# Performance work log

Hardware: AMD Instinct MI355X
Metric: run time of the kernel (lower is better)

## Reference

```python
import jax, jax.numpy as jnp
import numpy as np

C = 1024
H = 16
D = C // H

def setup_inputs() -> dict:
    key = jax.random.key(0)
    ks = jax.random.split(key, 12)
    s = 1.0 / np.sqrt(C)
    inp = {
        "Q": jax.random.normal(ks[0], (2, 1024, C), jnp.float32),
        "K_in": jax.random.normal(ks[1], (2, 4096, C), jnp.float32),
        "V_in": jax.random.normal(ks[2], (2, 4096, C), jnp.float32),
        "V_bias": jax.random.normal(ks[3], (2, 4096), jnp.float32),
        "Wq_w": jax.random.uniform(ks[4], (C, C), jnp.float32, -s, s),
        "Wq_b": jax.random.uniform(ks[5], (C,), jnp.float32, -s, s),
        "Wk_w": jax.random.uniform(ks[6], (C, C), jnp.float32, -s, s),
        "Wk_b": jax.random.uniform(ks[7], (C,), jnp.float32, -s, s),
        "Wv_w": jax.random.uniform(ks[8], (C, C), jnp.float32, -s, s),
        "Wv_b": jax.random.uniform(ks[9], (C,), jnp.float32, -s, s),
        "Wo_w": jax.random.uniform(ks[10], (C, C), jnp.float32, -s, s),
        "Wo_b": jax.random.uniform(ks[11], (C,), jnp.float32, -s, s),
    }
    return inp

def reference(Q, K_in, V_in, V_bias, Wq_w, Wq_b, Wk_w, Wk_b, Wv_w, Wv_b, Wo_w, Wo_b):
    B, Lq, _ = Q.shape
    Lk = K_in.shape[1]
    # linear projections (torch Linear: x @ W.T + b), split heads -> [B,H,L,D]
    q = (Q @ Wq_w.T + Wq_b).reshape(B, Lq, H, D).transpose(0, 2, 1, 3)
    k = (K_in @ Wk_w.T + Wk_b).reshape(B, Lk, H, D).transpose(0, 2, 1, 3)
    v = (V_in @ Wv_w.T + Wv_b).reshape(B, Lk, H, D).transpose(0, 2, 1, 3)
    scale = 1.0 / np.sqrt(D).astype(np.float32)
    logits = jnp.einsum("bhqd,bhkd->bhqk", q, k) * scale
    logits = logits + V_bias[:, None, None, :]  # per-key additive bias
    attn = jax.nn.softmax(logits, axis=-1)      # dropout p=0.0 (eval)
    out = jnp.einsum("bhqk,bhkd->bhqd", attn, v)
    out = out.transpose(0, 2, 1, 3).reshape(B, Lq, C)
    return out @ Wo_w.T + Wo_b
```

## Files before the change

### kernel.cpp

```cpp
#include <hip/hip_runtime.h>


typedef __attribute__((ext_vector_type(8))) __bf16 bf16x8;
typedef __attribute__((ext_vector_type(4))) float f32x4;
typedef __attribute__((ext_vector_type(16))) float f32x16;

#define LOG2E 1.44269504f

__device__ __forceinline__ unsigned short f2bf(float f) {
  union { float f; unsigned u; } v; v.f = f;
  unsigned r = v.u + 0x7fffu + ((v.u >> 16) & 1u);
  return (unsigned short)(r >> 16);
}
__device__ __forceinline__ unsigned short f2h(float x) {
  _Float16 h = (_Float16)x;
  return __builtin_bit_cast(unsigned short, h);
}
__device__ __forceinline__ float h2f(unsigned short u) {
  return (float)__builtin_bit_cast(_Float16, u);
}

__device__ __forceinline__ f32x4 mfma16(bf16x8 a, bf16x8 b, f32x4 c) {
  return __builtin_amdgcn_mfma_f32_16x16x32_bf16(a, b, c, 0, 0, 0);
}
__device__ __forceinline__ f32x16 mfma32(bf16x8 a, bf16x8 b, f32x16 c) {
  return __builtin_amdgcn_mfma_f32_32x32x16_bf16(a, b, c, 0, 0, 0);
}

__device__ __forceinline__ unsigned pk2(float lo, float hi) {
  unsigned short a = __builtin_bit_cast(unsigned short, (__bf16)lo);
  unsigned short b = __builtin_bit_cast(unsigned short, (__bf16)hi);
  return (unsigned)a | ((unsigned)b << 16);
}

template <typename T>
__device__ __forceinline__ void gload16(const T* g, T* l) {
  __builtin_amdgcn_global_load_lds(
      (const __attribute__((address_space(1))) void*)g,
      (__attribute__((address_space(3))) void*)l, 16, 0, 0);
}

struct Cvt4 {
  const float* src[4];
  unsigned short* dst[4];
};

__global__ __launch_bounds__(256) void cvt4_kernel(Cvt4 a, int n4) {
  const float4* s = (const float4*)a.src[blockIdx.y];
  unsigned short* d = a.dst[blockIdx.y];
  int stride = gridDim.x * blockDim.x;
  for (int i = blockIdx.x * blockDim.x + threadIdx.x; i < n4; i += stride) {
    float4 f = s[i];
    ushort4 u;
    u.x = f2bf(f.x); u.y = f2bf(f.y); u.z = f2bf(f.z); u.w = f2bf(f.w);
    ((ushort4*)d)[i] = u;
  }
}

__global__ __launch_bounds__(256) void prep_kb(const float* __restrict__ Vb,
                                               unsigned* __restrict__ kb) {
  const int i = blockIdx.x * 256 + threadIdx.x;
  const float x = Vb[i] * LOG2E;
  const unsigned short h = f2bf(x);
  union { unsigned u; float f; } hf; hf.u = (unsigned)h << 16;
  const unsigned short lo = f2bf(x - hf.f);
  kb[i] = (unsigned)h | ((unsigned)lo << 16);
}

template <int MODE, bool AF32>
__global__ __launch_bounds__(256) void gemm_bf16(
    const void* __restrict__ Ap, const unsigned short* __restrict__ W,
    const float* __restrict__ bias, void* __restrict__ outp,
    int M, int Llog2, float oscale) {
  constexpr int K = 1024, N = 1024;
  __shared__ unsigned short Alds[128][40];
  __shared__ unsigned short Blds[128][40];

  const int tid = threadIdx.x;
  const int wid = tid >> 6, l = tid & 63;
  const int wr = wid >> 1, wc = wid & 1;
  const int m0 = blockIdx.x * 128, n0 = blockIdx.y * 128;
  const int lg = l >> 4, lm = l & 15;

  const int crow = tid >> 2;
  const int ck8 = (tid & 3) * 8;

  const float* Af = (const float*)Ap;
  const unsigned short* Ab = (const unsigned short*)Ap;

  f32x4 acc[4][4] = {};
  uint4 ra[2], rb[2];

  auto loadA = [&](int kt, int half) -> uint4 {
    const int row = crow + half * 64;
    const long off = (long)(m0 + row) * K + kt * 32 + ck8;
    if constexpr (AF32) {
      float4 f0 = *(const float4*)(Af + off);
      float4 f1 = *(const float4*)(Af + off + 4);
      bf16x8 v;
      v[0] = (__bf16)f0.x; v[1] = (__bf16)f0.y;
      v[2] = (__bf16)f0.z; v[3] = (__bf16)f0.w;
      v[4] = (__bf16)f1.x; v[5] = (__bf16)f1.y;
      v[6] = (__bf16)f1.z; v[7] = (__bf16)f1.w;
      uint4 u;
      __builtin_memcpy(&u, &v, 16);
      return u;
    } else {
      return *(const uint4*)(Ab + off);
    }
  };
  auto loadB = [&](int kt, int half) -> uint4 {
    const int row = crow + half * 64;
    return *(const uint4*)(W + (long)(n0 + row) * K + kt * 32 + ck8);
  };

  ra[0] = loadA(0, 0); ra[1] = loadA(0, 1);
  rb[0] = loadB(0, 0); rb[1] = loadB(0, 1);

  for (int kt = 0; kt < K / 32; ++kt) {
    __syncthreads();
    *(uint4*)&Alds[crow][ck8] = ra[0];
    *(uint4*)&Alds[crow + 64][ck8] = ra[1];
    *(uint4*)&Blds[crow][ck8] = rb[0];
    *(uint4*)&Blds[crow + 64][ck8] = rb[1];
    __syncthreads();
    if (kt + 1 < K / 32) {
      ra[0] = loadA(kt + 1, 0); ra[1] = loadA(kt + 1, 1);
      rb[0] = loadB(kt + 1, 0); rb[1] = loadB(kt + 1, 1);
    }
    bf16x8 af[4], bfr[4];
#pragma unroll
    for (int i = 0; i < 4; ++i)
      af[i] = *(const bf16x8*)&Alds[wr * 64 + i * 16 + lm][lg * 8];
#pragma unroll
    for (int j = 0; j < 4; ++j)
      bfr[j] = *(const bf16x8*)&Blds[wc * 64 + j * 16 + lm][lg * 8];
#pragma unroll
    for (int i = 0; i < 4; ++i)
#pragma unroll
      for (int j = 0; j < 4; ++j) {
        if constexpr (MODE == 1)
          acc[i][j] = mfma16(bfr[i], af[j], acc[i][j]);
        else
          acc[i][j] = mfma16(af[i], bfr[j], acc[i][j]);
      }
  }

  const int rr = lg * 4;
  if constexpr (MODE == 0) {
    const int Lmask = (1 << Llog2) - 1;
    unsigned short* out = (unsigned short*)outp;
#pragma unroll
    for (int j = 0; j < 4; ++j) {
      const int n = n0 + wc * 64 + j * 16 + lm;
      const float bv = bias[n];
      const int h = n >> 6, d = n & 63;
#pragma unroll
      for (int i = 0; i < 4; ++i)
#pragma unroll
        for (int r = 0; r < 4; ++r) {
          const int m = m0 + wr * 64 + i * 16 + rr + r;
          const int b = m >> Llog2, li = m & Lmask;
          const long o = (((long)(b * 16 + h) << Llog2) + li) * 64 + d;
          out[o] = f2bf((acc[i][j][r] + bv) * oscale);
        }
    }
  } else if constexpr (MODE == 1) {
    unsigned short* out = (unsigned short*)outp;
#pragma unroll
    for (int i = 0; i < 4; ++i)
#pragma unroll
      for (int r = 0; r < 4; ++r) {
        const int n = n0 + wc * 64 + i * 16 + rr + r;
        const float bv = bias[n];
        const int h = n >> 6, d = n & 63;
#pragma unroll
        for (int j = 0; j < 4; ++j) {
          const int m = m0 + wr * 64 + j * 16 + lm;
          const int b = m >> 12, lk = m & 4095;
          const long o = ((long)((b * 16 + h) * 64 + d)) * 4096 + lk;
          out[o] = f2bf(acc[i][j][r] + bv);
        }
      }
  } else {
    float* out = (float*)outp;
#pragma unroll
    for (int j = 0; j < 4; ++j) {
      const int n = n0 + wc * 64 + j * 16 + lm;
      const float bv = bias[n];
#pragma unroll
      for (int i = 0; i < 4; ++i)
#pragma unroll
        for (int r = 0; r < 4; ++r) {
          const int m = m0 + wr * 64 + i * 16 + rr + r;
          out[(long)m * N + n] = acc[i][j][r] + bv;
        }
    }
  }
}

__global__ __launch_bounds__(256, 3) void attn32(
    const unsigned short* __restrict__ qh, const unsigned short* __restrict__ kh,
    const unsigned short* __restrict__ vT, const unsigned* __restrict__ kb,
    unsigned short* __restrict__ Oh, float* __restrict__ ml) {
  __shared__ unsigned short Klds[2][64][64];
  __shared__ unsigned short Vlds[2][64][64];

  const int tid = threadIdx.x;
  const int wid = tid >> 6, lane = tid & 63;
  const int lq = lane & 31, hi = lane >> 5;
  const int bh = blockIdx.x, qb = blockIdx.y, sp = blockIdx.z;
  const int b = bh >> 4;
  const int q = qb * 128 + wid * 32 + lq;
  const int kt0 = sp * 16;

  bf16x8 qr[4];
  {
    const unsigned short* qp = qh + ((long)bh * 1024 + q) * 64 + hi * 8;
#pragma unroll
    for (int dc = 0; dc < 4; ++dc) qr[dc] = *(const bf16x8*)(qp + dc * 16);
  }

  union uv { uint4 u; bf16x8 v; };
  uv ones; ones.u = make_uint4(0x3F803F80u, 0x3F803F80u, 0x3F803F80u, 0x3F803F80u);
  uv bq;   bq.u = make_uint4(hi ? 0u : 0x3F803F80u, 0u, 0u, 0u);

  auto swap23 = [](int r) { return (r & 0x33) | ((r & 4) << 1) | ((r & 8) >> 1); };
  const int r0 = wid * 16 + (lane >> 3), r1 = r0 + 8;
  const int s0 = ((lane & 7) ^ (r0 & 7)) * 8;
  const int s1 = ((lane & 7) ^ (r1 & 7)) * 8;
  const unsigned short* kg0 =
      kh + ((long)bh * 4096 + kt0 * 64 + swap23(r0)) * 64 + s0;
  const unsigned short* kg1 =
      kh + ((long)bh * 4096 + kt0 * 64 + swap23(r1)) * 64 + s1;
  const unsigned short* vg0 = vT + ((long)bh * 64 + r0) * 4096 + kt0 * 64 + s0;
  const unsigned short* vg1 = vT + ((long)bh * 64 + r1) * 4096 + kt0 * 64 + s1;
  const unsigned* kbp = kb + b * 4096 + kt0 * 64;
  const int kbkey = swap23(lq);

  auto issue = [&](int t, int buf) {
    gload16(kg0 + (long)t * 4096, &Klds[buf][wid * 16][0]);
    gload16(kg1 + (long)t * 4096, &Klds[buf][wid * 16 + 8][0]);
    gload16(vg0 + t * 64, &Vlds[buf][wid * 16][0]);
    gload16(vg1 + t * 64, &Vlds[buf][wid * 16 + 8][0]);
  };
  issue(0, 0);

  const int rsw = lq & 7;
  float mreg = -1e30f;
  f32x16 oa0 = {}, oa1 = {}, lacc = {};

  for (int t = 0; t < 16; ++t) {
    const int buf = t & 1;
    __syncthreads();
    if (t + 1 < 16) issue(t + 1, buf ^ 1);

    const unsigned kbw0 = kbp[t * 64 + kbkey];
    const unsigned kbw1 = kbp[t * 64 + 32 + kbkey];

    f32x16 sa0 = {}, sa1 = {};
    __builtin_amdgcn_s_setprio(1);
#pragma unroll
    for (int dc = 0; dc < 4; ++dc) {
      const int so = ((dc * 2 + hi) ^ rsw) * 8;
      bf16x8 kf0 = *(const bf16x8*)&Klds[buf][lq][so];
      bf16x8 kf1 = *(const bf16x8*)&Klds[buf][32 + lq][so];
      sa0 = mfma32(kf0, qr[dc], sa0);
      sa1 = mfma32(kf1, qr[dc], sa1);
    }
    {
      uv ka0, ka1;
      ka0.u = make_uint4(hi ? 0u : kbw0, 0u, 0u, 0u);
      ka1.u = make_uint4(hi ? 0u : kbw1, 0u, 0u, 0u);
      sa0 = mfma32(ka0.v, bq.v, sa0);
      sa1 = mfma32(ka1.v, bq.v, sa1);
    }
    __builtin_amdgcn_s_setprio(0);

    float p[32];
#pragma unroll
    for (int r = 0; r < 16; ++r) { p[r] = sa0[r]; p[16 + r] = sa1[r]; }

    float t8[8];
#pragma unroll
    for (int i = 0; i < 8; ++i)
      t8[i] = fmaxf(fmaxf(p[i], p[i + 8]), fmaxf(p[i + 16], p[i + 24]));
    float mx = fmaxf(fmaxf(fmaxf(t8[0], t8[1]), fmaxf(t8[2], t8[3])),
                     fmaxf(fmaxf(t8[4], t8[5]), fmaxf(t8[6], t8[7])));
    mx = fmaxf(mx, __shfl_xor(mx, 32));

    if (!__all(mx - mreg <= 8.0f)) {
      const float mnew = fmaxf(mreg, mx);
      const float al = __builtin_amdgcn_exp2f(mreg - mnew);
      mreg = mnew;
#pragma unroll
      for (int r = 0; r < 16; ++r) { oa0[r] *= al; oa1[r] *= al; }
      lacc[0] *= al;
    }
#pragma unroll
    for (int i = 0; i < 32; ++i) p[i] = __builtin_amdgcn_exp2f(p[i] - mreg);

    __builtin_amdgcn_s_setprio(1);
#pragma unroll
    for (int kc = 0; kc < 4; ++kc) {
      uv pu;
      pu.u = make_uint4(pk2(p[kc * 8 + 0], p[kc * 8 + 1]),
                        pk2(p[kc * 8 + 2], p[kc * 8 + 3]),
                        pk2(p[kc * 8 + 4], p[kc * 8 + 5]),
                        pk2(p[kc * 8 + 6], p[kc * 8 + 7]));
      const int so = ((kc * 2 + hi) ^ rsw) * 8;
      bf16x8 vf0 = *(const bf16x8*)&Vlds[buf][lq][so];
      bf16x8 vf1 = *(const bf16x8*)&Vlds[buf][32 + lq][so];
      oa0 = mfma32(vf0, pu.v, oa0);
      oa1 = mfma32(vf1, pu.v, oa1);
      lacc = mfma32(ones.v, pu.v, lacc);
    }
    __builtin_amdgcn_s_setprio(0);
  }

  const float lsum = lacc[0];
  const float inv = 1.0f / lsum;
  unsigned short* ob = Oh + (((long)sp * 32 + bh) * 1024 + q) * 64 + hi * 4;
#pragma unroll
  for (int g = 0; g < 4; ++g) {
    ushort4 u0, u1;
    u0.x = f2h(oa0[g * 4 + 0] * inv); u0.y = f2h(oa0[g * 4 + 1] * inv);
    u0.z = f2h(oa0[g * 4 + 2] * inv); u0.w = f2h(oa0[g * 4 + 3] * inv);
    u1.x = f2h(oa1[g * 4 + 0] * inv); u1.y = f2h(oa1[g * 4 + 1] * inv);
    u1.z = f2h(oa1[g * 4 + 2] * inv); u1.w = f2h(oa1[g * 4 + 3] * inv);
    *(ushort4*)(ob + g * 8) = u0;
    *(ushort4*)(ob + 32 + g * 8) = u1;
  }
  if (hi == 0)
    *(float2*)(ml + (((long)sp * 32 + bh) * 1024 + q) * 2) =
        make_float2(mreg, lsum);
}

__global__ __launch_bounds__(256) void combine4(
    const unsigned short* __restrict__ Oh, const float* __restrict__ ml,
    unsigned short* __restrict__ ao) {
  const int idx = blockIdx.x * 256 + threadIdx.x;
  const int bh = idx >> 10, q = idx & 1023;
  const int b = bh >> 4, h = bh & 15;
  float m[4], l[4];
#pragma unroll
  for (int i = 0; i < 4; ++i) {
    float2 t = *(const float2*)(ml + ((long)i * 32768 + idx) * 2);
    m[i] = t.x; l[i] = t.y;
  }
  const float mm = fmaxf(fmaxf(m[0], m[1]), fmaxf(m[2], m[3]));
  float w[4], wsum = 0.f;
#pragma unroll
  for (int i = 0; i < 4; ++i) {
    w[i] = l[i] * __builtin_amdgcn_exp2f(m[i] - mm);
    wsum += w[i];
  }
  const float inv = 1.0f / wsum;
#pragma unroll
  for (int i = 0; i < 4; ++i) w[i] *= inv;

  unsigned short* op = ao + ((long)b * 1024 + q) * 1024 + h * 64;
#pragma unroll
  for (int blk = 0; blk < 8; ++blk) {
    float acc[8] = {};
#pragma unroll
    for (int i = 0; i < 4; ++i) {
      uint4 u = *(const uint4*)(Oh + ((long)i * 32768 + idx) * 64 + blk * 8);
      const unsigned short* hs = (const unsigned short*)&u;
#pragma unroll
      for (int j = 0; j < 8; ++j) acc[j] += w[i] * h2f(hs[j]);
    }
    ushort4 o0, o1;
    o0.x = f2bf(acc[0]); o0.y = f2bf(acc[1]);
    o0.z = f2bf(acc[2]); o0.w = f2bf(acc[3]);
    o1.x = f2bf(acc[4]); o1.y = f2bf(acc[5]);
    o1.z = f2bf(acc[6]); o1.w = f2bf(acc[7]);
    *(ushort4*)(op + blk * 8) = o0;
    *(ushort4*)(op + blk * 8 + 4) = o1;
  }
}

extern "C" void kernel_launch(void* const* d_in, const int* in_sizes, int n_in,
                              void* d_out, int out_size, void* d_ws,
                              size_t ws_size, hipStream_t stream) {
  const float* Q = (const float*)d_in[0];
  const float* K_in = (const float*)d_in[1];
  const float* V_in = (const float*)d_in[2];
  const float* V_bias = (const float*)d_in[3];
  const float* Wq_w = (const float*)d_in[4];
  const float* Wq_b = (const float*)d_in[5];
  const float* Wk_w = (const float*)d_in[6];
  const float* Wk_b = (const float*)d_in[7];
  const float* Wv_w = (const float*)d_in[8];
  const float* Wv_b = (const float*)d_in[9];
  const float* Wo_w = (const float*)d_in[10];
  const float* Wo_b = (const float*)d_in[11];

  char* ws = (char*)d_ws;
  unsigned short* Wqb = (unsigned short*)(ws + (0l << 20));
  float* mlp = (float*)(ws + (0l << 20));
  unsigned short* Wkb = (unsigned short*)(ws + (2l << 20));
  unsigned short* Wvb = (unsigned short*)(ws + (4l << 20));
  unsigned short* Wob = (unsigned short*)(ws + (6l << 20));
  unsigned short* qhp = (unsigned short*)(ws + (8l << 20));
  unsigned short* khp = (unsigned short*)(ws + (12l << 20));
  unsigned short* vTp = (unsigned short*)(ws + (28l << 20));
  unsigned short* Ohp = (unsigned short*)(ws + (44l << 20));
  unsigned short* aop = (unsigned short*)(ws + (60l << 20));
  unsigned* kbp = (unsigned*)(ws + (64l << 20));

  Cvt4 c4;
  c4.src[0] = Wq_w; c4.src[1] = Wk_w; c4.src[2] = Wv_w; c4.src[3] = Wo_w;
  c4.dst[0] = Wqb;  c4.dst[1] = Wkb;  c4.dst[2] = Wvb;  c4.dst[3] = Wob;
  cvt4_kernel<<<dim3(256, 4), 256, 0, stream>>>(c4, (1024 * 1024) / 4);
  prep_kb<<<32, 256, 0, stream>>>(V_bias, kbp);

  gemm_bf16<0, true><<<dim3(16, 8), 256, 0, stream>>>(
      Q, Wqb, Wq_b, qhp, 2048, 10, 0.125f * LOG2E);
  gemm_bf16<0, true><<<dim3(64, 8), 256, 0, stream>>>(
      K_in, Wkb, Wk_b, khp, 8192, 12, 1.0f);
  gemm_bf16<1, true><<<dim3(64, 8), 256, 0, stream>>>(
      V_in, Wvb, Wv_b, vTp, 8192, 12, 1.0f);

  attn32<<<dim3(32, 8, 4), 256, 0, stream>>>(qhp, khp, vTp, kbp, Ohp, mlp);
  combine4<<<128, 256, 0, stream>>>(Ohp, mlp, aop);

  gemm_bf16<2, false><<<dim3(16, 8), 256, 0, stream>>>(
      aop, Wob, Wo_b, d_out, 2048, 0, 1.0f);
}
```

Measured before the change: 188.7 us.

## Restructure GEMM loads and double query tile per warp in attention

The projection GEMM now reads A straight from global memory into registers in MFMA fragment layout, and stages B with async global-to-LDS loads into a double buffer with a single barrier per k-step. A 64-row tile variant is added for the small Q and output GEMMs so they launch more blocks. The attention kernel gives each warp 64 queries as two interleaved 32-query groups that share K/V fragments, which improves reuse and overlaps softmax with MFMA. The row sum is now computed with a register reduction instead of an extra ones-vector MFMA. In exchange, register pressure rises, occupancy hints drop from 3 to 2, and the attention grid halves, leaving fewer waves on the GPU.

After: 285.4 us. 1.51x slower.

```diff
diff --git a/kernel.cpp b/kernel.cpp
--- a/kernel.cpp
+++ b/kernel.cpp
@@ -67,83 +67,95 @@
   kb[i] = (unsigned)h | ((unsigned)lo << 16);
 }
 
-template <int MODE, bool AF32>
-__global__ __launch_bounds__(256) void gemm_bf16(
+template <int MODE, bool AF32, int BM>
+__global__ __launch_bounds__(256, 2) void gemm_bf16(
     const void* __restrict__ Ap, const unsigned short* __restrict__ W,
     const float* __restrict__ bias, void* __restrict__ outp,
-    int M, int Llog2, float oscale) {
+    int Llog2, float oscale) {
   constexpr int K = 1024, N = 1024;
-  __shared__ unsigned short Alds[128][40];
-  __shared__ unsigned short Blds[128][40];
+  constexpr int NJ = (BM == 128) ? 4 : 2;
+  __shared__ unsigned short Blds[2][128][32];
 
   const int tid = threadIdx.x;
   const int wid = tid >> 6, l = tid & 63;
-  const int wr = wid >> 1, wc = wid & 1;
-  const int m0 = blockIdx.x * 128, n0 = blockIdx.y * 128;
   const int lg = l >> 4, lm = l & 15;
-
-  const int crow = tid >> 2;
-  const int ck8 = (tid & 3) * 8;
+  const int wr = (BM == 128) ? (wid >> 1) : 0;
+  const int wc = (BM == 128) ? (wid & 1) : wid;
+  const int m0 = blockIdx.x * BM, n0 = blockIdx.y * 128;
+  const int mbase = m0 + wr * 64;
+  const int nbase = (BM == 128) ? wc * 64 : wid * 32;
 
   const float* Af = (const float*)Ap;
   const unsigned short* Ab = (const unsigned short*)Ap;
 
-  f32x4 acc[4][4] = {};
-  uint4 ra[2], rb[2];
-
-  auto loadA = [&](int kt, int half) -> uint4 {
-    const int row = crow + half * 64;
-    const long off = (long)(m0 + row) * K + kt * 32 + ck8;
-    if constexpr (AF32) {
-      float4 f0 = *(const float4*)(Af + off);
-      float4 f1 = *(const float4*)(Af + off + 4);
-      bf16x8 v;
-      v[0] = (__bf16)f0.x; v[1] = (__bf16)f0.y;
-      v[2] = (__bf16)f0.z; v[3] = (__bf16)f0.w;
-      v[4] = (__bf16)f1.x; v[5] = (__bf16)f1.y;
-      v[6] = (__bf16)f1.z; v[7] = (__bf16)f1.w;
-      uint4 u;
-      __builtin_memcpy(&u, &v, 16);
-      return u;
-    } else {
-      return *(const uint4*)(Ab + off);
+  const int bidx = wid * 1024 + (tid & 63) * 16;
+  const int brow = bidx >> 6;
+  const int bcol = (bidx & 63) >> 1;
+  const unsigned short* bsrc0 = W + (long)(n0 + brow) * K + bcol;
+  const unsigned short* bsrc1 = W + (long)(n0 + 64 + brow) * K + bcol;
+
+  f32x4 acc[4][NJ] = {};
+  uint4 pa[4][2];
+
+  auto loadA = [&](int kt) {
+#pragma unroll
+    for (int i = 0; i < 4; ++i) {
+      const long off = (long)(mbase + i * 16 + lm) * K + kt * 32 + lg * 8;
+      if constexpr (AF32) {
+        pa[i][0] = *(const uint4*)(Af + off);
+        pa[i][1] = *(const uint4*)(Af + off + 4);
+      } else {
+        pa[i][0] = *(const uint4*)(Ab + off);
+      }
     }
   };
-  auto loadB = [&](int kt, int half) -> uint4 {
-    const int row = crow + half * 64;
-    return *(const uint4*)(W + (long)(n0 + row) * K + kt * 32 + ck8);
+  auto issueB = [&](int kt, int buf) {
+    gload16(bsrc0 + kt * 32, &Blds[buf][wid * 16][0]);
+    gload16(bsrc1 + kt * 32, &Blds[buf][64 + wid * 16][0]);
   };
 
-  ra[0] = loadA(0, 0); ra[1] = loadA(0, 1);
-  rb[0] = loadB(0, 0); rb[1] = loadB(0, 1);
+  issueB(0, 0);
+  loadA(0);
 
   for (int kt = 0; kt < K / 32; ++kt) {
+    const int buf = kt & 1;
     __syncthreads();
-    *(uint4*)&Alds[crow][ck8] = ra[0];
-    *(uint4*)&Alds[crow + 64][ck8] = ra[1];
-    *(uint4*)&Blds[crow][ck8] = rb[0];
-    *(uint4*)&Blds[crow + 64][ck8] = rb[1];
-    __syncthreads();
-    if (kt + 1 < K / 32) {
-      ra[0] = loadA(kt + 1, 0); ra[1] = loadA(kt + 1, 1);
-      rb[0] = loadB(kt + 1, 0); rb[1] = loadB(kt + 1, 1);
-    }
-    bf16x8 af[4], bfr[4];
+    if (kt + 1 < K / 32) issueB(kt + 1, buf ^ 1);
+
+    bf16x8 af[4];
+#pragma unroll
+    for (int i = 0; i < 4; ++i) {
+      if constexpr (AF32) {
+        union { uint4 u[2]; float f[8]; } t;
+        t.u[0] = pa[i][0]; t.u[1] = pa[i][1];
+        bf16x8 v;
+#pragma unroll
+        for (int e = 0; e < 8; ++e) v[e] = (__bf16)t.f[e];
+        af[i] = v;
+      } else {
+        union { uint4 u; bf16x8 v; } t;
+        t.u = pa[i][0];
+        af[i] = t.v;
+      }
+    }
+    if (kt + 1 < K / 32) loadA(kt + 1);
+
+    bf16x8 bfr[NJ];
+#pragma unroll
+    for (int j = 0; j < NJ; ++j)
+      bfr[j] = *(const bf16x8*)&Blds[buf][nbase + j * 16 + lm][lg * 8];
+
+    __builtin_amdgcn_s_setprio(1);
 #pragma unroll
     for (int i = 0; i < 4; ++i)
-      af[i] = *(const bf16x8*)&Alds[wr * 64 + i * 16 + lm][lg * 8];
-#pragma unroll
-    for (int j = 0; j < 4; ++j)
-      bfr[j] = *(const bf16x8*)&Blds[wc * 64 + j * 16 + lm][lg * 8];
-#pragma unroll
-    for (int i = 0; i < 4; ++i)
-#pragma unroll
-      for (int j = 0; j < 4; ++j) {
+#pragma unroll
+      for (int j = 0; j < NJ; ++j) {
         if constexpr (MODE == 1)
-          acc[i][j] = mfma16(bfr[i], af[j], acc[i][j]);
+          acc[i][j] = mfma16(bfr[j], af[i], acc[i][j]);
         else
           acc[i][j] = mfma16(af[i], bfr[j], acc[i][j]);
       }
+    __builtin_amdgcn_s_setprio(0);
   }
 
   const int rr = lg * 4;
@@ -151,15 +163,15 @@
     const int Lmask = (1 << Llog2) - 1;
     unsigned short* out = (unsigned short*)outp;
 #pragma unroll
-    for (int j = 0; j < 4; ++j) {
-      const int n = n0 + wc * 64 + j * 16 + lm;
+    for (int j = 0; j < NJ; ++j) {
+      const int n = n0 + nbase + j * 16 + lm;
       const float bv = bias[n];
       const int h = n >> 6, d = n & 63;
 #pragma unroll
       for (int i = 0; i < 4; ++i)
 #pragma unroll
         for (int r = 0; r < 4; ++r) {
-          const int m = m0 + wr * 64 + i * 16 + rr + r;
+          const int m = mbase + i * 16 + rr + r;
           const int b = m >> Llog2, li = m & Lmask;
           const long o = (((long)(b * 16 + h) << Llog2) + li) * 64 + d;
           out[o] = f2bf((acc[i][j][r] + bv) * oscale);
@@ -171,35 +183,35 @@
     for (int i = 0; i < 4; ++i)
 #pragma unroll
       for (int r = 0; r < 4; ++r) {
-        const int n = n0 + wc * 64 + i * 16 + rr + r;
+        const int n = n0 + nbase + i * 16 + rr + r;
         const float bv = bias[n];
         const int h = n >> 6, d = n & 63;
 #pragma unroll
         for (int j = 0; j < 4; ++j) {
-          const int m = m0 + wr * 64 + j * 16 + lm;
+          const int m = mbase + j * 16 + lm;
           const int b = m >> 12, lk = m & 4095;
           const long o = ((long)((b * 16 + h) * 64 + d)) * 4096 + lk;
-          out[o] = f2bf(acc[i][j][r] + bv);
+          out[o] = f2bf(acc[j][i][r] + bv);
         }
       }
   } else {
     float* out = (float*)outp;
 #pragma unroll
-    for (int j = 0; j < 4; ++j) {
-      const int n = n0 + wc * 64 + j * 16 + lm;
+    for (int j = 0; j < NJ; ++j) {
+      const int n = n0 + nbase + j * 16 + lm;
       const float bv = bias[n];
 #pragma unroll
       for (int i = 0; i < 4; ++i)
 #pragma unroll
         for (int r = 0; r < 4; ++r) {
-          const int m = m0 + wr * 64 + i * 16 + rr + r;
+          const int m = mbase + i * 16 + rr + r;
           out[(long)m * N + n] = acc[i][j][r] + bv;
         }
     }
   }
 }
 
-__global__ __launch_bounds__(256, 3) void attn32(
+__global__ __launch_bounds__(256, 2) void attn64(
     const unsigned short* __restrict__ qh, const unsigned short* __restrict__ kh,
     const unsigned short* __restrict__ vT, const unsigned* __restrict__ kb,
     unsigned short* __restrict__ Oh, float* __restrict__ ml) {
@@ -211,19 +223,21 @@
   const int lq = lane & 31, hi = lane >> 5;
   const int bh = blockIdx.x, qb = blockIdx.y, sp = blockIdx.z;
   const int b = bh >> 4;
-  const int q = qb * 128 + wid * 32 + lq;
+  const int qA = qb * 256 + wid * 64 + lq;
   const int kt0 = sp * 16;
 
-  bf16x8 qr[4];
+  bf16x8 qrA[4], qrB[4];
   {
-    const unsigned short* qp = qh + ((long)bh * 1024 + q) * 64 + hi * 8;
-#pragma unroll
-    for (int dc = 0; dc < 4; ++dc) qr[dc] = *(const bf16x8*)(qp + dc * 16);
+    const unsigned short* qp = qh + ((long)bh * 1024 + qA) * 64 + hi * 8;
+#pragma unroll
+    for (int dc = 0; dc < 4; ++dc) {
+      qrA[dc] = *(const bf16x8*)(qp + dc * 16);
+      qrB[dc] = *(const bf16x8*)(qp + 32 * 64 + dc * 16);
+    }
   }
 
   union uv { uint4 u; bf16x8 v; };
-  uv ones; ones.u = make_uint4(0x3F803F80u, 0x3F803F80u, 0x3F803F80u, 0x3F803F80u);
-  uv bq;   bq.u = make_uint4(hi ? 0u : 0x3F803F80u, 0u, 0u, 0u);
+  uv bq; bq.u = make_uint4(hi ? 0u : 0x3F803F80u, 0u, 0u, 0u);
 
   auto swap23 = [](int r) { return (r & 0x33) | ((r & 4) << 1) | ((r & 8) >> 1); };
   const int r0 = wid * 16 + (lane >> 3), r1 = r0 + 8;
@@ -247,40 +261,15 @@
   issue(0, 0);
 
   const int rsw = lq & 7;
-  float mreg = -1e30f;
-  f32x16 oa0 = {}, oa1 = {}, lacc = {};
-
-  for (int t = 0; t < 16; ++t) {
-    const int buf = t & 1;
-    __syncthreads();
-    if (t + 1 < 16) issue(t + 1, buf ^ 1);
-
-    const unsigned kbw0 = kbp[t * 64 + kbkey];
-    const unsigned kbw1 = kbp[t * 64 + 32 + kbkey];
-
-    f32x16 sa0 = {}, sa1 = {};
-    __builtin_amdgcn_s_setprio(1);
-#pragma unroll
-    for (int dc = 0; dc < 4; ++dc) {
-      const int so = ((dc * 2 + hi) ^ rsw) * 8;
-      bf16x8 kf0 = *(const bf16x8*)&Klds[buf][lq][so];
-      bf16x8 kf1 = *(const bf16x8*)&Klds[buf][32 + lq][so];
-      sa0 = mfma32(kf0, qr[dc], sa0);
-      sa1 = mfma32(kf1, qr[dc], sa1);
-    }
-    {
-      uv ka0, ka1;
-      ka0.u = make_uint4(hi ? 0u : kbw0, 0u, 0u, 0u);
-      ka1.u = make_uint4(hi ? 0u : kbw1, 0u, 0u, 0u);
-      sa0 = mfma32(ka0.v, bq.v, sa0);
-      sa1 = mfma32(ka1.v, bq.v, sa1);
-    }
-    __builtin_amdgcn_s_setprio(0);
-
+  float mA = -1e30f, mB = -1e30f, lA = 0.f, lB = 0.f;
+  f32x16 oaA0 = {}, oaA1 = {}, oaB0 = {}, oaB1 = {};
+  uv puA[4], puB[4];
+
+  auto softmax = [&](f32x16& sx0, f32x16& sx1, float& mreg, float& lreg,
+                     f32x16& o0, f32x16& o1, uv* pu) {
     float p[32];
 #pragma unroll
-    for (int r = 0; r < 16; ++r) { p[r] = sa0[r]; p[16 + r] = sa1[r]; }
-
+    for (int r = 0; r < 16; ++r) { p[r] = sx0[r]; p[16 + r] = sx1[r]; }
     float t8[8];
 #pragma unroll
     for (int i = 0; i < 8; ++i)
@@ -288,52 +277,118 @@
     float mx = fmaxf(fmaxf(fmaxf(t8[0], t8[1]), fmaxf(t8[2], t8[3])),
                      fmaxf(fmaxf(t8[4], t8[5]), fmaxf(t8[6], t8[7])));
     mx = fmaxf(mx, __shfl_xor(mx, 32));
-
     if (!__all(mx - mreg <= 8.0f)) {
       const float mnew = fmaxf(mreg, mx);
       const float al = __builtin_amdgcn_exp2f(mreg - mnew);
       mreg = mnew;
 #pragma unroll
-      for (int r = 0; r < 16; ++r) { oa0[r] *= al; oa1[r] *= al; }
-      lacc[0] *= al;
+      for (int r = 0; r < 16; ++r) { o0[r] *= al; o1[r] *= al; }
+      lreg *= al;
     }
 #pragma unroll
     for (int i = 0; i < 32; ++i) p[i] = __builtin_amdgcn_exp2f(p[i] - mreg);
-
+    float s16[16];
+#pragma unroll
+    for (int i = 0; i < 16; ++i) s16[i] = p[i] + p[i + 16];
+#pragma unroll
+    for (int s = 8; s > 0; s >>= 1)
+#pragma unroll
+      for (int i = 0; i < 8; ++i)
+        if (i < s) s16[i] += s16[i + s];
+    lreg += s16[0] + __shfl_xor(s16[0], 32);
+#pragma unroll
+    for (int kc = 0; kc < 4; ++kc)
+      pu[kc].u = make_uint4(pk2(p[kc * 8 + 0], p[kc * 8 + 1]),
+                            pk2(p[kc * 8 + 2], p[kc * 8 + 3]),
+                            pk2(p[kc * 8 + 4], p[kc * 8 + 5]),
+                            pk2(p[kc * 8 + 6], p[kc * 8 + 7]));
+  };
+
+  for (int t = 0; t < 16; ++t) {
+    const int buf = t & 1;
+    __syncthreads();
+    if (t + 1 < 16) issue(t + 1, buf ^ 1);
+
+    uv ka0, ka1;
+    ka0.u = make_uint4(hi ? 0u : kbp[t * 64 + kbkey], 0u, 0u, 0u);
+    ka1.u = make_uint4(hi ? 0u : kbp[t * 64 + 32 + kbkey], 0u, 0u, 0u);
+
+    bf16x8 kf0[4], kf1[4];
+#pragma unroll
+    for (int dc = 0; dc < 4; ++dc) {
+      const int so = ((dc * 2 + hi) ^ rsw) * 8;
+      kf0[dc] = *(const bf16x8*)&Klds[buf][lq][so];
+      kf1[dc] = *(const bf16x8*)&Klds[buf][32 + lq][so];
+    }
+
+    f32x16 sa0 = {}, sa1 = {};
     __builtin_amdgcn_s_setprio(1);
 #pragma unroll
+    for (int dc = 0; dc < 4; ++dc) {
+      sa0 = mfma32(kf0[dc], qrA[dc], sa0);
+      sa1 = mfma32(kf1[dc], qrA[dc], sa1);
+    }
+    sa0 = mfma32(ka0.v, bq.v, sa0);
+    sa1 = mfma32(ka1.v, bq.v, sa1);
+    __builtin_amdgcn_s_setprio(0);
+    softmax(sa0, sa1, mA, lA, oaA0, oaA1, puA);
+
+    f32x16 sb0 = {}, sb1 = {};
+    __builtin_amdgcn_s_setprio(1);
+#pragma unroll
+    for (int dc = 0; dc < 4; ++dc) {
+      sb0 = mfma32(kf0[dc], qrB[dc], sb0);
+      sb1 = mfma32(kf1[dc], qrB[dc], sb1);
+    }
+    sb0 = mfma32(ka0.v, bq.v, sb0);
+    sb1 = mfma32(ka1.v, bq.v, sb1);
+    __builtin_amdgcn_s_setprio(0);
+
+    bf16x8 vf0[4], vf1[4];
+#pragma unroll
     for (int kc = 0; kc < 4; ++kc) {
-      uv pu;
-      pu.u = make_uint4(pk2(p[kc * 8 + 0], p[kc * 8 + 1]),
-                        pk2(p[kc * 8 + 2], p[kc * 8 + 3]),
-                        pk2(p[kc * 8 + 4], p[kc * 8 + 5]),
-                        pk2(p[kc * 8 + 6], p[kc * 8 + 7]));
       const int so = ((kc * 2 + hi) ^ rsw) * 8;
-      bf16x8 vf0 = *(const bf16x8*)&Vlds[buf][lq][so];
-      bf16x8 vf1 = *(const bf16x8*)&Vlds[buf][32 + lq][so];
-      oa0 = mfma32(vf0, pu.v, oa0);
-      oa1 = mfma32(vf1, pu.v, oa1);
-      lacc = mfma32(ones.v, pu.v, lacc);
+      vf0[kc] = *(const bf16x8*)&Vlds[buf][lq][so];
+      vf1[kc] = *(const bf16x8*)&Vlds[buf][32 + lq][so];
+    }
+    softmax(sb0, sb1, mB, lB, oaB0, oaB1, puB);
+
+    __builtin_amdgcn_s_setprio(1);
+#pragma unroll
+    for (int kc = 0; kc < 4; ++kc) {
+      oaA0 = mfma32(vf0[kc], puA[kc].v, oaA0);
+      oaA1 = mfma32(vf1[kc], puA[kc].v, oaA1);
+      oaB0 = mfma32(vf0[kc], puB[kc].v, oaB0);
+      oaB1 = mfma32(vf1[kc], puB[kc].v, oaB1);
     }
     __builtin_amdgcn_s_setprio(0);
   }
 
-  const float lsum = lacc[0];
-  const float inv = 1.0f / lsum;
-  unsigned short* ob = Oh + (((long)sp * 32 + bh) * 1024 + q) * 64 + hi * 4;
+  const float invA = 1.0f / lA, invB = 1.0f / lB;
+  unsigned short* obA = Oh + (((long)sp * 32 + bh) * 1024 + qA) * 64 + hi * 4;
+  unsigned short* obB = obA + 32 * 64;
 #pragma unroll
   for (int g = 0; g < 4; ++g) {
-    ushort4 u0, u1;
-    u0.x = f2h(oa0[g * 4 + 0] * inv); u0.y = f2h(oa0[g * 4 + 1] * inv);
-    u0.z = f2h(oa0[g * 4 + 2] * inv); u0.w = f2h(oa0[g * 4 + 3] * inv);
-    u1.x = f2h(oa1[g * 4 + 0] * inv); u1.y = f2h(oa1[g * 4 + 1] * inv);
-    u1.z = f2h(oa1[g * 4 + 2] * inv); u1.w = f2h(oa1[g * 4 + 3] * inv);
-    *(ushort4*)(ob + g * 8) = u0;
-    *(ushort4*)(ob + 32 + g * 8) = u1;
-  }
-  if (hi == 0)
-    *(float2*)(ml + (((long)sp * 32 + bh) * 1024 + q) * 2) =
-        make_float2(mreg, lsum);
+    ushort4 u;
+    u.x = f2h(oaA0[g * 4 + 0] * invA); u.y = f2h(oaA0[g * 4 + 1] * invA);
+    u.z = f2h(oaA0[g * 4 + 2] * invA); u.w = f2h(oaA0[g * 4 + 3] * invA);
+    *(ushort4*)(obA + g * 8) = u;
+    u.x = f2h(oaA1[g * 4 + 0] * invA); u.y = f2h(oaA1[g * 4 + 1] * invA);
+    u.z = f2h(oaA1[g * 4 + 2] * invA); u.w = f2h(oaA1[g * 4 + 3] * invA);
+    *(ushort4*)(obA + 32 + g * 8) = u;
+    u.x = f2h(oaB0[g * 4 + 0] * invB); u.y = f2h(oaB0[g * 4 + 1] * invB);
+    u.z = f2h(oaB0[g * 4 + 2] * invB); u.w = f2h(oaB0[g * 4 + 3] * invB);
+    *(ushort4*)(obB + g * 8) = u;
+    u.x = f2h(oaB1[g * 4 + 0] * invB); u.y = f2h(oaB1[g * 4 + 1] * invB);
+    u.z = f2h(oaB1[g * 4 + 2] * invB); u.w = f2h(oaB1[g * 4 + 3] * invB);
+    *(ushort4*)(obB + 32 + g * 8) = u;
+  }
+  if (hi == 0) {
+    *(float2*)(ml + (((long)sp * 32 + bh) * 1024 + qA) * 2) =
+        make_float2(mA, lA);
+    *(float2*)(ml + (((long)sp * 32 + bh) * 1024 + qA + 32) * 2) =
+        make_float2(mB, lB);
+  }
 }
 
 __global__ __launch_bounds__(256) void combine4(
@@ -415,16 +470,16 @@
   cvt4_kernel<<<dim3(256, 4), 256, 0, stream>>>(c4, (1024 * 1024) / 4);
   prep_kb<<<32, 256, 0, stream>>>(V_bias, kbp);
 
-  gemm_bf16<0, true><<<dim3(16, 8), 256, 0, stream>>>(
-      Q, Wqb, Wq_b, qhp, 2048, 10, 0.125f * LOG2E);
-  gemm_bf16<0, true><<<dim3(64, 8), 256, 0, stream>>>(
-      K_in, Wkb, Wk_b, khp, 8192, 12, 1.0f);
-  gemm_bf16<1, true><<<dim3(64, 8), 256, 0, stream>>>(
-      V_in, Wvb, Wv_b, vTp, 8192, 12, 1.0f);
-
-  attn32<<<dim3(32, 8, 4), 256, 0, stream>>>(qhp, khp, vTp, kbp, Ohp, mlp);
+  gemm_bf16<0, true, 64><<<dim3(32, 8), 256, 0, stream>>>(
+      Q, Wqb, Wq_b, qhp, 10, 0.125f * LOG2E);
+  gemm_bf16<0, true, 128><<<dim3(64, 8), 256, 0, stream>>>(
+      K_in, Wkb, Wk_b, khp, 12, 1.0f);
+  gemm_bf16<1, true, 128><<<dim3(64, 8), 256, 0, stream>>>(
+      V_in, Wvb, Wv_b, vTp, 12, 1.0f);
+
+  attn64<<<dim3(32, 4, 4), 256, 0, stream>>>(qhp, khp, vTp, kbp, Ohp, mlp);
   combine4<<<128, 256, 0, stream>>>(Ohp, mlp, aop);
 
-  gemm_bf16<2, false><<<dim3(16, 8), 256, 0, stream>>>(
-      aop, Wob, Wo_b, d_out, 2048, 0, 1.0f);
-}
+  gemm_bf16<2, false, 64><<<dim3(32, 8), 256, 0, stream>>>(
+      aop, Wob, Wo_b, d_out, 0, 1.0f);
+}
```
